# Kernel tuning notes

Measured on AMD Instinct MI355X. Metric: run time of the kernel, lower is better.

Reference implementation:

```python
import jax, jax.numpy as jnp
import numpy as np

DIM = 2048
N_HEADS = 16
HEAD_DIM = DIM // N_HEADS  # 128
HIDDEN = 8192
EPS = 1e-6
NEG = -1e9


def rmsnorm(x, w):
    xf = x.astype(jnp.float32)
    y = xf * jax.lax.rsqrt(jnp.mean(xf * xf, axis=-1, keepdims=True) + EPS)
    return y.astype(x.dtype) * w


def apply_rope(x, cos, sin):
    # x: [B,S,H,Hd]; cos/sin: [S,Hd//2] -> broadcast [1,S,1,Hd//2]
    xf = x.astype(jnp.float32)
    xr = xf[..., 0::2]
    xi = xf[..., 1::2]
    c = cos[None, :, None, :]
    s = sin[None, :, None, :]
    or_ = xr * c - xi * s
    oi_ = xr * s + xi * c
    out = jnp.stack([or_, oi_], axis=-1).reshape(x.shape)
    return out.astype(x.dtype)


def setup_inputs() -> dict:
    key = jax.random.key(0)
    ks = jax.random.split(key, 10)
    B, S = 1, 2048
    x = jax.random.normal(ks[0], (B, S, DIM), dtype=jnp.float32)
    # RoPE frequencies (Llama-style, theta=10000)
    inv_freq = 1.0 / (10000.0 ** (jnp.arange(0, HEAD_DIM, 2, dtype=jnp.float32) / HEAD_DIM))
    angles = jnp.arange(S, dtype=jnp.float32)[:, None] * inv_freq[None, :]  # [S, Hd//2]
    freqs_cos = jnp.cos(angles)
    freqs_sin = jnp.sin(angles)
    # causal additive mask [1,1,S,S]
    mask = jnp.where(jnp.tril(jnp.ones((S, S), dtype=bool)), 0.0, NEG).astype(jnp.float32)[None, None]
    sc = 0.02
    wq = jax.random.normal(ks[1], (DIM, DIM), dtype=jnp.float32) * sc
    wk = jax.random.normal(ks[2], (DIM, DIM), dtype=jnp.float32) * sc
    wv = jax.random.normal(ks[3], (DIM, DIM), dtype=jnp.float32) * sc
    wo = jax.random.normal(ks[4], (DIM, DIM), dtype=jnp.float32) * sc
    w1 = jax.random.normal(ks[5], (DIM, HIDDEN), dtype=jnp.float32) * sc
    w2 = jax.random.normal(ks[6], (HIDDEN, DIM), dtype=jnp.float32) * sc
    w3 = jax.random.normal(ks[7], (DIM, HIDDEN), dtype=jnp.float32) * sc
    attn_norm_w = jnp.ones((DIM,), dtype=jnp.float32)
    ffn_norm_w = jnp.ones((DIM,), dtype=jnp.float32)
    return {"x": x, "freqs_cos": freqs_cos, "freqs_sin": freqs_sin, "mask": mask,
            "wq": wq, "wk": wk, "wv": wv, "wo": wo, "w1": w1, "w2": w2, "w3": w3,
            "attn_norm_w": attn_norm_w, "ffn_norm_w": ffn_norm_w}


def reference(x, freqs_cos, freqs_sin, mask, wq, wk, wv, wo, w1, w2, w3, attn_norm_w, ffn_norm_w):
    B, S, D = x.shape
    # --- attention (pre-norm) ---
    hn = rmsnorm(x, attn_norm_w)
    q = (hn @ wq).reshape(B, S, N_HEADS, HEAD_DIM)
    k = (hn @ wk).reshape(B, S, N_HEADS, HEAD_DIM)
    v = (hn @ wv).reshape(B, S, N_HEADS, HEAD_DIM)
    q = apply_rope(q, freqs_cos, freqs_sin)
    k = apply_rope(k, freqs_cos, freqs_sin)
    scores = jnp.einsum('bqhd,bkhd->bhqk', q, k) / (HEAD_DIM ** 0.5) + mask
    attn = jax.nn.softmax(scores.astype(jnp.float32), axis=-1).astype(q.dtype)
    ctx = jnp.einsum('bhqk,bkhd->bqhd', attn, v).reshape(B, S, D)
    h = x + ctx @ wo
    # --- SwiGLU FFN (pre-norm) ---
    fn = rmsnorm(h, ffn_norm_w)
    ff = (jax.nn.silu(fn @ w1) * (fn @ w3)) @ w2
    return h + ff
```

## Files before the change

kernel.cpp:

```cpp
#include <hip/hip_runtime.h>
#include <hip/hip_bf16.h>

#define DIM 2048
#define HEAD_DIM 128
#define N_HEADS 16
#define SEQ 2048
#define HID 8192
#define SQKV 6144

typedef short bf16x8 __attribute__((ext_vector_type(8)));
typedef float f32x4 __attribute__((ext_vector_type(4)));
using bf16 = __hip_bfloat16;

#define MFMA16(a, b, c) __builtin_amdgcn_mfma_f32_16x16x32_bf16(a, b, c, 0, 0, 0)

__device__ __forceinline__ unsigned short f2bu(float f) {
    union { bf16 b; unsigned short u; } cv;
    cv.b = __float2bfloat16(f);
    return cv.u;
}

__device__ __forceinline__ void gl16(const void* g, void* l) {
    __builtin_amdgcn_global_load_lds(
        (const __attribute__((address_space(1))) unsigned int*)g,
        (__attribute__((address_space(3))) unsigned int*)l, 16, 0, 0);
}

__global__ __launch_bounds__(256) void rmsnorm_bf16_k(
    const float* __restrict__ x, const float* __restrict__ w, bf16* __restrict__ y)
{
    const int row = blockIdx.x;
    const int tid = threadIdx.x;
    const float* xr = x + (size_t)row * DIM;
    float4 v0 = ((const float4*)xr)[tid];
    float4 v1 = ((const float4*)xr)[tid + 256];
    float ss = v0.x*v0.x + v0.y*v0.y + v0.z*v0.z + v0.w*v0.w
             + v1.x*v1.x + v1.y*v1.y + v1.z*v1.z + v1.w*v1.w;
    for (int o = 32; o > 0; o >>= 1) ss += __shfl_down(ss, o);
    __shared__ float red[4];
    if ((tid & 63) == 0) red[tid >> 6] = ss;
    __syncthreads();
    float tot = red[0] + red[1] + red[2] + red[3];
    float r = rsqrtf(tot * (1.0f / DIM) + 1e-6f);
    float4 w0 = ((const float4*)w)[tid];
    float4 w1 = ((const float4*)w)[tid + 256];
    ushort4 o0, o1;
    o0.x = f2bu(v0.x * r * w0.x); o0.y = f2bu(v0.y * r * w0.y);
    o0.z = f2bu(v0.z * r * w0.z); o0.w = f2bu(v0.w * r * w0.w);
    o1.x = f2bu(v1.x * r * w1.x); o1.y = f2bu(v1.y * r * w1.y);
    o1.z = f2bu(v1.z * r * w1.z); o1.w = f2bu(v1.w * r * w1.w);
    ushort4* yr = (ushort4*)(y + (size_t)row * DIM);
    yr[tid] = o0;
    yr[tid + 256] = o1;
}

__global__ __launch_bounds__(256) void rmsnorm4_k(
    const float* __restrict__ part, const float* __restrict__ x,
    const float* __restrict__ w, float* __restrict__ hout, bf16* __restrict__ y)
{
    const int row = blockIdx.x;
    const int tid = threadIdx.x;
    const size_t base = (size_t)row * DIM;
    const size_t SP = (size_t)SEQ * DIM;
    float4 r0, r1;
    float ss = 0.0f;
    {
        float4 a  = ((const float4*)(x + base))[tid];
        float4 p0 = ((const float4*)(part + base))[tid];
        float4 p1 = ((const float4*)(part + SP + base))[tid];
        float4 p2 = ((const float4*)(part + 2 * SP + base))[tid];
        float4 p3 = ((const float4*)(part + 3 * SP + base))[tid];
        r0.x = a.x + ((p0.x + p1.x) + (p2.x + p3.x));
        r0.y = a.y + ((p0.y + p1.y) + (p2.y + p3.y));
        r0.z = a.z + ((p0.z + p1.z) + (p2.z + p3.z));
        r0.w = a.w + ((p0.w + p1.w) + (p2.w + p3.w));
        ((float4*)(hout + base))[tid] = r0;
        ss += r0.x*r0.x + r0.y*r0.y + r0.z*r0.z + r0.w*r0.w;
    }
    {
        const int t2 = tid + 256;
        float4 a  = ((const float4*)(x + base))[t2];
        float4 p0 = ((const float4*)(part + base))[t2];
        float4 p1 = ((const float4*)(part + SP + base))[t2];
        float4 p2 = ((const float4*)(part + 2 * SP + base))[t2];
        float4 p3 = ((const float4*)(part + 3 * SP + base))[t2];
        r1.x = a.x + ((p0.x + p1.x) + (p2.x + p3.x));
        r1.y = a.y + ((p0.y + p1.y) + (p2.y + p3.y));
        r1.z = a.z + ((p0.z + p1.z) + (p2.z + p3.z));
        r1.w = a.w + ((p0.w + p1.w) + (p2.w + p3.w));
        ((float4*)(hout + base))[t2] = r1;
        ss += r1.x*r1.x + r1.y*r1.y + r1.z*r1.z + r1.w*r1.w;
    }
    for (int o = 32; o > 0; o >>= 1) ss += __shfl_down(ss, o);
    __shared__ float red[4];
    if ((tid & 63) == 0) red[tid >> 6] = ss;
    __syncthreads();
    float tot = red[0] + red[1] + red[2] + red[3];
    float r = rsqrtf(tot * (1.0f / DIM) + 1e-6f);
    float4 w0 = ((const float4*)w)[tid];
    float4 w1 = ((const float4*)w)[tid + 256];
    ushort4 o0, o1;
    o0.x = f2bu(r0.x * r * w0.x); o0.y = f2bu(r0.y * r * w0.y);
    o0.z = f2bu(r0.z * r * w0.z); o0.w = f2bu(r0.w * r * w0.w);
    o1.x = f2bu(r1.x * r * w1.x); o1.y = f2bu(r1.y * r * w1.y);
    o1.z = f2bu(r1.z * r * w1.z); o1.w = f2bu(r1.w * r * w1.w);
    ushort4* yr = (ushort4*)(y + base);
    yr[tid] = o0;
    yr[tid + 256] = o1;
}

__global__ __launch_bounds__(256) void reduce4_k(
    const float* __restrict__ part, const float* __restrict__ h, float* __restrict__ out)
{
    const size_t i = (size_t)blockIdx.x * 256 + threadIdx.x;
    const size_t SP4 = (size_t)SEQ * DIM / 4;
    float4 a  = ((const float4*)h)[i];
    float4 p0 = ((const float4*)part)[i];
    float4 p1 = ((const float4*)part)[i + SP4];
    float4 p2 = ((const float4*)part)[i + 2 * SP4];
    float4 p3 = ((const float4*)part)[i + 3 * SP4];
    float4 r;
    r.x = a.x + ((p0.x + p1.x) + (p2.x + p3.x));
    r.y = a.y + ((p0.y + p1.y) + (p2.y + p3.y));
    r.z = a.z + ((p0.z + p1.z) + (p2.z + p3.z));
    r.w = a.w + ((p0.w + p1.w) + (p2.w + p3.w));
    ((float4*)out)[i] = r;
}

__global__ __launch_bounds__(256) void convT_f32_bf16_k(
    const float* __restrict__ in, bf16* __restrict__ out, int R, int C)
{
    __shared__ float t[32][33];
    const int tx = threadIdx.x, ty = threadIdx.y;
    const int x0 = blockIdx.x * 32, y0 = blockIdx.y * 32;
#pragma unroll
    for (int i = 0; i < 4; ++i)
        t[ty + i * 8][tx] = in[(size_t)(y0 + ty + i * 8) * C + x0 + tx];
    __syncthreads();
#pragma unroll
    for (int i = 0; i < 4; ++i)
        out[(size_t)(x0 + ty + i * 8) * R + y0 + tx] = __float2bfloat16(t[tx][ty + i * 8]);
}

__global__ __launch_bounds__(256) void convT3_f32_bf16_k(
    const float* __restrict__ wq, const float* __restrict__ wk,
    const float* __restrict__ wv, bf16* __restrict__ out)
{
    const int z = blockIdx.z;
    const float* in = z == 0 ? wq : (z == 1 ? wk : wv);
    bf16* o = out + (size_t)z * DIM * DIM;
    __shared__ float t[32][33];
    const int tx = threadIdx.x, ty = threadIdx.y;
    const int x0 = blockIdx.x * 32, y0 = blockIdx.y * 32;
#pragma unroll
    for (int i = 0; i < 4; ++i)
        t[ty + i * 8][tx] = in[(size_t)(y0 + ty + i * 8) * DIM + x0 + tx];
    __syncthreads();
#pragma unroll
    for (int i = 0; i < 4; ++i)
        o[(size_t)(x0 + ty + i * 8) * DIM + y0 + tx] = __float2bfloat16(t[tx][ty + i * 8]);
}

__global__ __launch_bounds__(256) void transpose_bf16_k(
    const bf16* __restrict__ in, int istride, bf16* __restrict__ out)
{
    __shared__ unsigned short t[32][33];
    const int tx = threadIdx.x, ty = threadIdx.y;
    const int x = blockIdx.x * 32 + tx;
    const int y0 = blockIdx.y * 32;
    const unsigned short* inu = (const unsigned short*)in;
    unsigned short* outu = (unsigned short*)out;
#pragma unroll
    for (int i = 0; i < 4; ++i)
        t[ty + i * 8][tx] = inu[(size_t)(y0 + ty + i * 8) * istride + x];
    __syncthreads();
    const int x2 = blockIdx.y * 32 + tx;
    const int y2 = blockIdx.x * 32;
#pragma unroll
    for (int i = 0; i < 4; ++i)
        outu[(size_t)(y2 + ty + i * 8) * SEQ + x2] = t[tx][ty + i * 8];
}

__global__ __launch_bounds__(256) void rope_qk_k(
    bf16* __restrict__ q, bf16* __restrict__ k,
    const float* __restrict__ cosb, const float* __restrict__ sinb)
{
    const int gid = blockIdx.x * 256 + threadIdx.x;
    const int s = gid >> 10;
    const int p = gid & 1023;
    const int h = p >> 6, j = p & 63;
    const size_t off = (size_t)s * SQKV + h * HEAD_DIM + 2 * j;
    const float c = cosb[s * 64 + j], sn = sinb[s * 64 + j];
    float xr = __bfloat162float(q[off]), xi = __bfloat162float(q[off + 1]);
    q[off]     = __float2bfloat16(xr * c - xi * sn);
    q[off + 1] = __float2bfloat16(xr * sn + xi * c);
    xr = __bfloat162float(k[off]); xi = __bfloat162float(k[off + 1]);
    k[off]     = __float2bfloat16(xr * c - xi * sn);
    k[off + 1] = __float2bfloat16(xr * sn + xi * c);
}

template <int EP>
__global__ __launch_bounds__(512, 1) void gemm256_k(
    const bf16* __restrict__ A, const bf16* __restrict__ Bt, const bf16* __restrict__ Bt2,
    bf16* __restrict__ Cb, float* __restrict__ Pf,
    int M, int N, int K, int gx, int ntile, int Ks)
{
    extern __shared__ char smem[];
    const int t512 = threadIdx.x;
    const int w = t512 >> 6, lane = t512 & 63;
    const int lr = lane & 15, lg = lane >> 4;
    const int wm = w >> 2, wn = w & 3;
    const int bofs = (wn & 1) * 64;
    const int swz = (lr & 7) << 4;

    const int nwg = gridDim.x;
    const int q8 = nwg >> 3, r8 = nwg & 7;
    const int xcd = blockIdx.x & 7, seqq = blockIdx.x >> 3;
    const int wgid = (xcd < r8 ? xcd * (q8 + 1) : r8 * (q8 + 1) + (xcd - r8) * q8) + seqq;
    const int split = wgid / ntile;
    const int tile = wgid % ntile;
    const int grp = tile / (4 * gx), rem = tile % (4 * gx);
    const int m0 = (grp * 4 + (rem & 3)) * 256, n0 = (rem >> 2) * 256;
    const int kb0 = split * Ks;
    const int niter = Ks >> 7;

    const bf16* aS[2][2]; const bf16* bS[2][2];
    int sOff[2];
#pragma unroll
    for (int c = 0; c < 2; ++c) {
        const int s = (c * 512 + t512) * 16;
        const int pp = s ^ (((s >> 7) & 7) << 4);
        const int row = pp >> 7, colE = (pp & 127) >> 1;
        sOff[c] = s;
#pragma unroll
        for (int hs = 0; hs < 2; ++hs) {
            aS[hs][c] = A + (size_t)(m0 + hs * 128 + row) * K + kb0 + colE;
            const int rg = n0 + hs * 128 + row;
            if (EP == 4) {
                const int g = rg >> 4;
                const bf16* src = (g & 1) ? Bt2 : Bt;
                const int j = ((g >> 1) << 4) + (rg & 15);
                bS[hs][c] = src + (size_t)j * K + kb0 + colE;
            } else {
                bS[hs][c] = Bt + (size_t)rg * K + kb0 + colE;
            }
        }
    }
    auto stA = [&](int buf, int kt, int hs) {
        char* base = smem + (buf * 2 + hs) * 16384;
        gl16(aS[hs][0] + (kt << 6), base + sOff[0]);
        gl16(aS[hs][1] + (kt << 6), base + sOff[1]);
    };
    auto stB = [&](int buf, int kt, int hs) {
        char* base = smem + 65536 + (buf * 2 + hs) * 16384;
        gl16(bS[hs][0] + (kt << 6), base + sOff[0]);
        gl16(bS[hs][1] + (kt << 6), base + sOff[1]);
    };

    const char* A0m = smem + (0 * 2 + wm) * 16384;
    const char* A1m = smem + (1 * 2 + wm) * 16384;
    const char* B0m = smem + 65536 + (0 * 2 + (wn >> 1)) * 16384;
    const char* B1m = smem + 65536 + (1 * 2 + (wn >> 1)) * 16384;

    f32x4 acc[8][4] = {};
    bf16x8 bfr[4][2];
    bf16x8 x0, x1, x2, x3;

#define SBAR __builtin_amdgcn_s_barrier()
#define LGKM0 do { asm volatile("s_waitcnt lgkmcnt(0)" ::: "memory"); \
                   __builtin_amdgcn_sched_barrier(0); } while (0)
#define WVM(n) do { asm volatile("s_waitcnt vmcnt(" #n ")" ::: "memory"); \
                    __builtin_amdgcn_sched_barrier(0); } while (0)
#define LDA4(base, mf0) do { \
    x0 = *(const bf16x8*)((base) + (((mf0) * 16 + lr) * 128) + ((lg * 16) ^ swz)); \
    x1 = *(const bf16x8*)((base) + (((mf0) * 16 + lr) * 128) + ((64 + lg * 16) ^ swz)); \
    x2 = *(const bf16x8*)((base) + ((((mf0) + 1) * 16 + lr) * 128) + ((lg * 16) ^ swz)); \
    x3 = *(const bf16x8*)((base) + ((((mf0) + 1) * 16 + lr) * 128) + ((64 + lg * 16) ^ swz)); \
    } while (0)
#define LDB8(base) do { \
    _Pragma("unroll") \
    for (int nf = 0; nf < 4; ++nf) { \
        bfr[nf][0] = *(const bf16x8*)((base) + ((bofs + nf * 16 + lr) * 128) + ((lg * 16) ^ swz)); \
        bfr[nf][1] = *(const bf16x8*)((base) + ((bofs + nf * 16 + lr) * 128) + ((64 + lg * 16) ^ swz)); \
    } } while (0)
#define MFMA_PH(mf0) do { \
    __builtin_amdgcn_s_setprio(1); \
    _Pragma("unroll") \
    for (int nf = 0; nf < 4; ++nf) { \
        acc[(mf0)][nf]     = MFMA16(x0, bfr[nf][0], acc[(mf0)][nf]); \
        acc[(mf0)][nf]     = MFMA16(x1, bfr[nf][1], acc[(mf0)][nf]); \
        acc[(mf0) + 1][nf] = MFMA16(x2, bfr[nf][0], acc[(mf0) + 1][nf]); \
        acc[(mf0) + 1][nf] = MFMA16(x3, bfr[nf][1], acc[(mf0) + 1][nf]); \
    } \
    __builtin_amdgcn_s_setprio(0); } while (0)

    stB(0, 0, 0); stB(0, 0, 1); stA(0, 0, 0); stA(0, 0, 1);
    stB(1, 1, 0); stB(1, 1, 1);
    WVM(4);
    SBAR;

    for (int t = 0; t < niter; ++t) {
        const bool pf = (t + 1 < niter);
        const int k1 = 2 * t + 1, k2 = 2 * t + 2, k3 = 2 * t + 3;

        LDB8(B0m);
        LDA4(A0m, 0);
        stA(1, k1, 0);
        SBAR; LGKM0; MFMA_PH(0); SBAR;
        LDA4(A0m, 2);
        stA(1, k1, 1);
        SBAR; LGKM0; MFMA_PH(2); SBAR;
        LDA4(A0m, 4);
        if (pf) stB(0, k2, 0);
        SBAR; LGKM0; MFMA_PH(4); SBAR;
        if (pf) { WVM(2); } else { WVM(0); }
        LDA4(A0m, 6);
        if (pf) stB(0, k2, 1);
        SBAR; LGKM0; MFMA_PH(6); SBAR;
        LDB8(B1m);
        LDA4(A1m, 0);
        if (pf) stA(0, k2, 0);
        SBAR; LGKM0; MFMA_PH(0); SBAR;
        LDA4(A1m, 2);
        if (pf) stA(0, k2, 1);
        SBAR; LGKM0; MFMA_PH(2); SBAR;
        LDA4(A1m, 4);
        if (pf) stB(1, k3, 0);
        SBAR; LGKM0; MFMA_PH(4); SBAR;
        if (pf) WVM(2);
        LDA4(A1m, 6);
        if (pf) stB(1, k3, 1);
        SBAR; LGKM0; MFMA_PH(6); SBAR;
    }
#undef SBAR
#undef LGKM0
#undef WVM
#undef LDA4
#undef LDB8
#undef MFMA_PH

    if (EP == 4) {
        const int jb = (n0 >> 1) + wn * 32;
        const int NH = N >> 1;
#pragma unroll
        for (int mf = 0; mf < 8; ++mf)
#pragma unroll
            for (int pp = 0; pp < 4; pp += 2) {
                const int row = m0 + wm * 128 + mf * 16 + lg * 4;
                const int j = jb + (pp >> 1) * 16 + lr;
#pragma unroll
                for (int r = 0; r < 4; ++r) {
                    const float a = acc[mf][pp][r];
                    const float b = acc[mf][pp + 1][r];
                    const float s = a / (1.0f + __expf(-a));
                    Cb[(size_t)(row + r) * NH + j] = __float2bfloat16(s * b);
                }
            }
    } else {
        float* pf_base = Pf + (size_t)split * M * N;
#pragma unroll
        for (int mf = 0; mf < 8; ++mf)
#pragma unroll
            for (int nf = 0; nf < 4; ++nf) {
                const int row = m0 + wm * 128 + mf * 16 + lg * 4;
                const int col = n0 + wn * 64 + nf * 16 + lr;
#pragma unroll
                for (int r = 0; r < 4; ++r) {
                    const size_t idx = (size_t)(row + r) * N + col;
                    const float v = acc[mf][nf][r];
                    if (EP == 0) Cb[idx] = __float2bfloat16(v);
                    else         pf_base[idx] = v;
                }
            }
    }
}

__global__ __launch_bounds__(256) void attn_fwd_k(
    const bf16* __restrict__ qkv, const bf16* __restrict__ vT, bf16* __restrict__ ctx)
{
    const int tid = threadIdx.x;
    const int w = tid >> 6, lane = tid & 63;
    const int lr = lane & 15, lg = lane >> 4;
    const int h = blockIdx.y;
    const int qidx = (blockIdx.y < 8) ? blockIdx.x : (31 - blockIdx.x);
    const int q0b = qidx * 64;
    const int nt = qidx + 1;

    __shared__ __align__(16) unsigned short Kt[2][64 * 128];
    __shared__ __align__(16) unsigned short Vt[2][128 * 64];
    __shared__ __align__(16) unsigned short Pp[4][16 * 64];

    const char* kbase = (const char*)(qkv + DIM + h * HEAD_DIM);
    const char* vbase = (const char*)(vT + (size_t)h * HEAD_DIM * SEQ);

    const int krow_c = tid >> 4;
    const int kcolB  = (tid & 15) * 16;
    const int vrow_c = tid >> 3;
    const int vcolB  = (tid & 7) * 16;

    auto stage = [&](int buf, int kb) {
#pragma unroll
        for (int c = 0; c < 4; ++c) {
            const int r = c * 16 + krow_c;
            gl16(kbase + (size_t)(kb + r) * (SQKV * 2) + (kcolB ^ ((r & 7) << 4)),
                 &Kt[buf][c * 2048 + tid * 8]);
        }
#pragma unroll
        for (int c = 0; c < 4; ++c) {
            const int r = c * 32 + vrow_c;
            gl16(vbase + (size_t)r * (SEQ * 2) + kb * 2 + (vcolB ^ ((r & 7) << 4)),
                 &Vt[buf][c * 2048 + tid * 8]);
        }
    };

    bf16x8 qf[4];
    const bf16* qrow = qkv + (size_t)(q0b + w * 16 + lr) * SQKV + h * HEAD_DIM;
#pragma unroll
    for (int dt = 0; dt < 4; ++dt)
        qf[dt] = *(const bf16x8*)(qrow + dt * 32 + lg * 8);

    f32x4 o[8] = {};
    float m[4], l[4];
#pragma unroll
    for (int j = 0; j < 4; ++j) { m[j] = -3e38f; l[j] = 0.0f; }
    const float scale = 0.08838834764831845f;

    stage(0, 0);
    __syncthreads();

    int cur = 0;
    for (int t = 0; t < nt; ++t) {
        const int kb = t * 64;
        if (t + 1 < nt) stage(cur ^ 1, kb + 64);

        f32x4 s[4] = {};
        __builtin_amdgcn_s_setprio(1);
#pragma unroll
        for (int ss = 0; ss < 4; ++ss) {
            const int r = ss * 16 + lr;
            const int sw = (r & 7) << 3;
#pragma unroll
            for (int dt = 0; dt < 4; ++dt) {
                bf16x8 kf = *(const bf16x8*)&Kt[cur][r * 128 + ((dt * 32 + lg * 8) ^ sw)];
                s[ss] = MFMA16(qf[dt], kf, s[ss]);
            }
        }
        __builtin_amdgcn_s_setprio(0);

        float al[4];
#pragma unroll
        for (int j = 0; j < 4; ++j) {
            const int qi = q0b + w * 16 + lg * 4 + j;
            const int prow = lg * 4 + j;
            const int psw = (prow & 7) << 3;
            float a[4];
#pragma unroll
            for (int ss = 0; ss < 4; ++ss)
                a[ss] = s[ss][j] * scale + ((kb + ss * 16 + lr) > qi ? -1e9f : 0.0f);
            float mx = fmaxf(fmaxf(a[0], a[1]), fmaxf(a[2], a[3]));
            mx = fmaxf(mx, __shfl_xor(mx, 1));
            mx = fmaxf(mx, __shfl_xor(mx, 2));
            mx = fmaxf(mx, __shfl_xor(mx, 4));
            mx = fmaxf(mx, __shfl_xor(mx, 8));
            const float mn = fmaxf(m[j], mx);
            const float asc = __expf(m[j] - mn);
            float e0 = __expf(a[0] - mn), e1 = __expf(a[1] - mn);
            float e2 = __expf(a[2] - mn), e3 = __expf(a[3] - mn);
            float rs = (e0 + e1) + (e2 + e3);
            rs += __shfl_xor(rs, 1); rs += __shfl_xor(rs, 2);
            rs += __shfl_xor(rs, 4); rs += __shfl_xor(rs, 8);
            l[j] = l[j] * asc + rs;
            m[j] = mn;
            al[j] = asc;
            Pp[w][prow * 64 + ((lr)      ^ psw)] = f2bu(e0);
            Pp[w][prow * 64 + ((16 + lr) ^ psw)] = f2bu(e1);
            Pp[w][prow * 64 + ((32 + lr) ^ psw)] = f2bu(e2);
            Pp[w][prow * 64 + ((48 + lr) ^ psw)] = f2bu(e3);
        }
#pragma unroll
        for (int d2 = 0; d2 < 8; ++d2)
#pragma unroll
            for (int j = 0; j < 4; ++j) o[d2][j] *= al[j];

        asm volatile("s_waitcnt lgkmcnt(0)" ::: "memory");
        __builtin_amdgcn_sched_barrier(0);
        const int asw = (lr & 7) << 3;
        bf16x8 pa0 = *(const bf16x8*)&Pp[w][lr * 64 + ((lg * 8)      ^ asw)];
        bf16x8 pa1 = *(const bf16x8*)&Pp[w][lr * 64 + ((32 + lg * 8) ^ asw)];

        __builtin_amdgcn_s_setprio(1);
#pragma unroll
        for (int d2 = 0; d2 < 8; ++d2) {
            const int rv = d2 * 16 + lr;
            const int vsw = (rv & 7) << 3;
            bf16x8 vf0 = *(const bf16x8*)&Vt[cur][rv * 64 + ((lg * 8)      ^ vsw)];
            bf16x8 vf1 = *(const bf16x8*)&Vt[cur][rv * 64 + ((32 + lg * 8) ^ vsw)];
            o[d2] = MFMA16(pa0, vf0, o[d2]);
            o[d2] = MFMA16(pa1, vf1, o[d2]);
        }
        __builtin_amdgcn_s_setprio(0);

        __syncthreads();
        cur ^= 1;
    }

#pragma unroll
    for (int j = 0; j < 4; ++j) {
        const float inv = 1.0f / l[j];
        bf16* dst = ctx + (size_t)(q0b + w * 16 + lg * 4 + j) * DIM + h * HEAD_DIM + lr;
#pragma unroll
        for (int d2 = 0; d2 < 8; ++d2)
            dst[d2 * 16] = __float2bfloat16(o[d2][j] * inv);
    }
}

extern "C" void kernel_launch(void* const* d_in, const int* in_sizes, int n_in,
                              void* d_out, int out_size, void* d_ws, size_t ws_size,
                              hipStream_t stream)
{
    const float* x   = (const float*)d_in[0];
    const float* fc  = (const float*)d_in[1];
    const float* fs  = (const float*)d_in[2];
    const float* wq  = (const float*)d_in[4];
    const float* wk  = (const float*)d_in[5];
    const float* wv  = (const float*)d_in[6];
    const float* wo  = (const float*)d_in[7];
    const float* w1  = (const float*)d_in[8];
    const float* w2  = (const float*)d_in[9];
    const float* w3  = (const float*)d_in[10];
    const float* anw = (const float*)d_in[11];
    const float* fnw = (const float*)d_in[12];
    float* out = (float*)d_out;

    char* p = (char*)d_ws;
    auto alloc = [&](size_t n) { char* r = p; p += (n + 255) & ~(size_t)255; return r; };
    bf16* wT  = (bf16*)alloc((size_t)HID * DIM * 2);
    bf16* hn  = (bf16*)alloc((size_t)SEQ * DIM * 2);
    bf16* qkv = (bf16*)alloc((size_t)SEQ * SQKV * 2);
    bf16* vt  = (bf16*)alloc((size_t)SEQ * DIM * 2);
    bf16* ctx = (bf16*)alloc((size_t)SEQ * DIM * 2);
    bf16* fn  = (bf16*)alloc((size_t)SEQ * DIM * 2);
    float* h  = (float*)alloc((size_t)SEQ * DIM * 4);
    bf16* g   = (bf16*)alloc((size_t)SEQ * HID * 2);
    float* sk = (float*)alloc((size_t)4 * SEQ * DIM * 4);
    bf16* w3T = hn;

    const dim3 tb32(32, 8);
    const int LDS256 = 131072;
    (void)hipFuncSetAttribute((const void*)gemm256_k<0>,
        hipFuncAttributeMaxDynamicSharedMemorySize, LDS256);
    (void)hipFuncSetAttribute((const void*)gemm256_k<3>,
        hipFuncAttributeMaxDynamicSharedMemorySize, LDS256);
    (void)hipFuncSetAttribute((const void*)gemm256_k<4>,
        hipFuncAttributeMaxDynamicSharedMemorySize, LDS256);

    rmsnorm_bf16_k<<<SEQ, 256, 0, stream>>>(x, anw, hn);

    convT3_f32_bf16_k<<<dim3(DIM / 32, DIM / 32, 3), tb32, 0, stream>>>(wq, wk, wv, wT);
    gemm256_k<0><<<(SEQ / 256) * (SQKV / 256), 512, LDS256, stream>>>(
        hn, wT, nullptr, qkv, nullptr, SEQ, SQKV, DIM, SQKV / 256, (SEQ / 256) * (SQKV / 256), DIM);

    rope_qk_k<<<(SEQ * 1024) / 256, 256, 0, stream>>>(qkv, qkv + DIM, fc, fs);
    transpose_bf16_k<<<dim3(DIM / 32, SEQ / 32), tb32, 0, stream>>>(qkv + 2 * DIM, SQKV, vt);

    attn_fwd_k<<<dim3(SEQ / 64, N_HEADS), 256, 0, stream>>>(qkv, vt, ctx);

    convT_f32_bf16_k<<<dim3(DIM / 32, DIM / 32), tb32, 0, stream>>>(wo, wT, DIM, DIM);
    gemm256_k<3><<<(SEQ / 256) * (DIM / 256) * 4, 512, LDS256, stream>>>(
        ctx, wT, nullptr, nullptr, sk, SEQ, DIM, DIM, DIM / 256, (SEQ / 256) * (DIM / 256), 512);
    rmsnorm4_k<<<SEQ, 256, 0, stream>>>(sk, x, fnw, h, fn);

    convT_f32_bf16_k<<<dim3(HID / 32, DIM / 32), tb32, 0, stream>>>(w1, wT, DIM, HID);
    convT_f32_bf16_k<<<dim3(HID / 32, DIM / 32), tb32, 0, stream>>>(w3, w3T, DIM, HID);
    gemm256_k<4><<<(SEQ / 256) * ((2 * HID) / 256), 512, LDS256, stream>>>(
        fn, wT, w3T, g, nullptr, SEQ, 2 * HID, DIM, (2 * HID) / 256,
        (SEQ / 256) * ((2 * HID) / 256), DIM);

    convT_f32_bf16_k<<<dim3(DIM / 32, HID / 32), tb32, 0, stream>>>(w2, wT, HID, DIM);
    gemm256_k<3><<<(SEQ / 256) * (DIM / 256) * 4, 512, LDS256, stream>>>(
        g, wT, nullptr, nullptr, sk, SEQ, DIM, HID, DIM / 256, (SEQ / 256) * (DIM / 256), 2048);
    reduce4_k<<<(SEQ * DIM / 4) / 256, 256, 0, stream>>>(sk, h, out);
}
```

Measured before the change: 491.4 us.

## Pair causal query tiles in one attention block to share K/V staging

The attention kernel now runs 512 threads per block. Two groups of four waves each take complementary query tiles (qidx and 31-qidx), so one block covers a balanced pair and the K/V tiles staged in LDS are shared by both. V is no longer double-buffered; it is loaded each iteration and waited on before the PV step, while K stays double-buffered. Waves whose tile is already finished idle through the barriers. Separately, the GEMM main loop gains a partial lgkmcnt(8) wait before the first barrier of each half-iteration.

```diff
diff --git a/kernel.cpp b/kernel.cpp
--- a/kernel.cpp
+++ b/kernel.cpp
@@ -269,6 +269,8 @@
 #define SBAR __builtin_amdgcn_s_barrier()
 #define LGKM0 do { asm volatile("s_waitcnt lgkmcnt(0)" ::: "memory"); \
                    __builtin_amdgcn_sched_barrier(0); } while (0)
+#define LGKM8 do { asm volatile("s_waitcnt lgkmcnt(8)" ::: "memory"); \
+                   __builtin_amdgcn_sched_barrier(0); } while (0)
 #define WVM(n) do { asm volatile("s_waitcnt vmcnt(" #n ")" ::: "memory"); \
                     __builtin_amdgcn_sched_barrier(0); } while (0)
 #define LDA4(base, mf0) do { \
@@ -306,6 +308,7 @@
         LDB8(B0m);
         LDA4(A0m, 0);
         stA(1, k1, 0);
+        LGKM8;
         SBAR; LGKM0; MFMA_PH(0); SBAR;
         LDA4(A0m, 2);
         stA(1, k1, 1);
@@ -320,6 +323,7 @@
         LDB8(B1m);
         LDA4(A1m, 0);
         if (pf) stA(0, k2, 0);
+        LGKM8;
         SBAR; LGKM0; MFMA_PH(0); SBAR;
         LDA4(A1m, 2);
         if (pf) stA(0, k2, 1);
@@ -334,6 +338,7 @@
     }
 #undef SBAR
 #undef LGKM0
+#undef LGKM8
 #undef WVM
 #undef LDA4
 #undef LDB8
@@ -375,20 +380,23 @@
     }
 }
 
-__global__ __launch_bounds__(256) void attn_fwd_k(
+__global__ __launch_bounds__(512) void attn_fwd_k(
     const bf16* __restrict__ qkv, const bf16* __restrict__ vT, bf16* __restrict__ ctx)
 {
     const int tid = threadIdx.x;
-    const int w = tid >> 6, lane = tid & 63;
+    const int w8 = tid >> 6, lane = tid & 63;
     const int lr = lane & 15, lg = lane >> 4;
+    const int w = w8 & 3, tsel = w8 >> 2;
     const int h = blockIdx.y;
-    const int qidx = (blockIdx.y < 8) ? blockIdx.x : (31 - blockIdx.x);
+    const int bx = blockIdx.x;
+    const int qidx = tsel ? (31 - bx) : bx;
     const int q0b = qidx * 64;
-    const int nt = qidx + 1;
+    const int myNt = qidx + 1;
+    const int nt = 32 - bx;
 
     __shared__ __align__(16) unsigned short Kt[2][64 * 128];
-    __shared__ __align__(16) unsigned short Vt[2][128 * 64];
-    __shared__ __align__(16) unsigned short Pp[4][16 * 64];
+    __shared__ __align__(16) unsigned short Vt[128 * 64];
+    __shared__ __align__(16) unsigned short Pp[8][16 * 64];
 
     const char* kbase = (const char*)(qkv + DIM + h * HEAD_DIM);
     const char* vbase = (const char*)(vT + (size_t)h * HEAD_DIM * SEQ);
@@ -398,20 +406,22 @@
     const int vrow_c = tid >> 3;
     const int vcolB  = (tid & 7) * 16;
 
-    auto stage = [&](int buf, int kb) {
-#pragma unroll
-        for (int c = 0; c < 4; ++c) {
-            const int r = c * 16 + krow_c;
+    auto stageK = [&](int buf, int kb) {
+#pragma unroll
+        for (int c = 0; c < 2; ++c) {
+            const int r = c * 32 + krow_c;
             gl16(kbase + (size_t)(kb + r) * (SQKV * 2) + (kcolB ^ ((r & 7) << 4)),
-                 &Kt[buf][c * 2048 + tid * 8]);
-        }
-#pragma unroll
-        for (int c = 0; c < 4; ++c) {
-            const int r = c * 32 + vrow_c;
-            gl16(vbase + (size_t)r * (SEQ * 2) + kb * 2 + (vcolB ^ ((r & 7) << 4)),
-                 &Vt[buf][c * 2048 + tid * 8]);
+                 &Kt[buf][c * 4096 + tid * 8]);
         }
     };
+    auto stageV = [&](int kb) {
+#pragma unroll
+        for (int c = 0; c < 2; ++c) {
+            const int r = c * 64 + vrow_c;
+            gl16(vbase + (size_t)r * (SEQ * 2) + kb * 2 + (vcolB ^ ((r & 7) << 4)),
+                 &Vt[c * 4096 + tid * 8]);
+        }
+    };
 
     bf16x8 qf[4];
     const bf16* qrow = qkv + (size_t)(q0b + w * 16 + lr) * SQKV + h * HEAD_DIM;
@@ -425,82 +435,96 @@
     for (int j = 0; j < 4; ++j) { m[j] = -3e38f; l[j] = 0.0f; }
     const float scale = 0.08838834764831845f;
 
-    stage(0, 0);
-    __syncthreads();
+    stageK(0, 0);
+    asm volatile("s_waitcnt vmcnt(0)" ::: "memory");
+    __builtin_amdgcn_sched_barrier(0);
+    __builtin_amdgcn_s_barrier();
 
     int cur = 0;
     for (int t = 0; t < nt; ++t) {
         const int kb = t * 64;
-        if (t + 1 < nt) stage(cur ^ 1, kb + 64);
-
-        f32x4 s[4] = {};
-        __builtin_amdgcn_s_setprio(1);
-#pragma unroll
-        for (int ss = 0; ss < 4; ++ss) {
-            const int r = ss * 16 + lr;
-            const int sw = (r & 7) << 3;
-#pragma unroll
-            for (int dt = 0; dt < 4; ++dt) {
-                bf16x8 kf = *(const bf16x8*)&Kt[cur][r * 128 + ((dt * 32 + lg * 8) ^ sw)];
-                s[ss] = MFMA16(qf[dt], kf, s[ss]);
+        const bool pf = (t + 1 < nt);
+        stageV(kb);
+        if (pf) stageK(cur ^ 1, kb + 64);
+        const bool act = (t < myNt);
+
+        if (act) {
+            f32x4 s[4] = {};
+            __builtin_amdgcn_s_setprio(1);
+#pragma unroll
+            for (int ss = 0; ss < 4; ++ss) {
+                const int r = ss * 16 + lr;
+                const int sw = (r & 7) << 3;
+#pragma unroll
+                for (int dt = 0; dt < 4; ++dt) {
+                    bf16x8 kf = *(const bf16x8*)&Kt[cur][r * 128 + ((dt * 32 + lg * 8) ^ sw)];
+                    s[ss] = MFMA16(qf[dt], kf, s[ss]);
+                }
             }
+            __builtin_amdgcn_s_setprio(0);
+
+            float al[4];
+#pragma unroll
+            for (int j = 0; j < 4; ++j) {
+                const int qi = q0b + w * 16 + lg * 4 + j;
+                const int prow = lg * 4 + j;
+                const int psw = (prow & 7) << 3;
+                float a[4];
+#pragma unroll
+                for (int ss = 0; ss < 4; ++ss)
+                    a[ss] = s[ss][j] * scale + ((kb + ss * 16 + lr) > qi ? -1e9f : 0.0f);
+                float mx = fmaxf(fmaxf(a[0], a[1]), fmaxf(a[2], a[3]));
+                mx = fmaxf(mx, __shfl_xor(mx, 1));
+                mx = fmaxf(mx, __shfl_xor(mx, 2));
+                mx = fmaxf(mx, __shfl_xor(mx, 4));
+                mx = fmaxf(mx, __shfl_xor(mx, 8));
+                const float mn = fmaxf(m[j], mx);
+                const float asc = __expf(m[j] - mn);
+                float e0 = __expf(a[0] - mn), e1 = __expf(a[1] - mn);
+                float e2 = __expf(a[2] - mn), e3 = __expf(a[3] - mn);
+                float rs = (e0 + e1) + (e2 + e3);
+                rs += __shfl_xor(rs, 1); rs += __shfl_xor(rs, 2);
+                rs += __shfl_xor(rs, 4); rs += __shfl_xor(rs, 8);
+                l[j] = l[j] * asc + rs;
+                m[j] = mn;
+                al[j] = asc;
+                Pp[w8][prow * 64 + ((lr)      ^ psw)] = f2bu(e0);
+                Pp[w8][prow * 64 + ((16 + lr) ^ psw)] = f2bu(e1);
+                Pp[w8][prow * 64 + ((32 + lr) ^ psw)] = f2bu(e2);
+                Pp[w8][prow * 64 + ((48 + lr) ^ psw)] = f2bu(e3);
+            }
+#pragma unroll
+            for (int d2 = 0; d2 < 8; ++d2)
+#pragma unroll
+                for (int j = 0; j < 4; ++j) o[d2][j] *= al[j];
         }
-        __builtin_amdgcn_s_setprio(0);
-
-        float al[4];
-#pragma unroll
-        for (int j = 0; j < 4; ++j) {
-            const int qi = q0b + w * 16 + lg * 4 + j;
-            const int prow = lg * 4 + j;
-            const int psw = (prow & 7) << 3;
-            float a[4];
-#pragma unroll
-            for (int ss = 0; ss < 4; ++ss)
-                a[ss] = s[ss][j] * scale + ((kb + ss * 16 + lr) > qi ? -1e9f : 0.0f);
-            float mx = fmaxf(fmaxf(a[0], a[1]), fmaxf(a[2], a[3]));
-            mx = fmaxf(mx, __shfl_xor(mx, 1));
-            mx = fmaxf(mx, __shfl_xor(mx, 2));
-            mx = fmaxf(mx, __shfl_xor(mx, 4));
-            mx = fmaxf(mx, __shfl_xor(mx, 8));
-            const float mn = fmaxf(m[j], mx);
-            const float asc = __expf(m[j] - mn);
-            float e0 = __expf(a[0] - mn), e1 = __expf(a[1] - mn);
-            float e2 = __expf(a[2] - mn), e3 = __expf(a[3] - mn);
-            float rs = (e0 + e1) + (e2 + e3);
-            rs += __shfl_xor(rs, 1); rs += __shfl_xor(rs, 2);
-            rs += __shfl_xor(rs, 4); rs += __shfl_xor(rs, 8);
-            l[j] = l[j] * asc + rs;
-            m[j] = mn;
-            al[j] = asc;
-            Pp[w][prow * 64 + ((lr)      ^ psw)] = f2bu(e0);
-            Pp[w][prow * 64 + ((16 + lr) ^ psw)] = f2bu(e1);
-            Pp[w][prow * 64 + ((32 + lr) ^ psw)] = f2bu(e2);
-            Pp[w][prow * 64 + ((48 + lr) ^ psw)] = f2bu(e3);
+
+        if (pf) { asm volatile("s_waitcnt vmcnt(2)" ::: "memory"); }
+        else    { asm volatile("s_waitcnt vmcnt(0)" ::: "memory"); }
+        __builtin_amdgcn_sched_barrier(0);
+        __builtin_amdgcn_s_barrier();
+
+        if (act) {
+            asm volatile("s_waitcnt lgkmcnt(0)" ::: "memory");
+            __builtin_amdgcn_sched_barrier(0);
+            const int asw = (lr & 7) << 3;
+            bf16x8 pa0 = *(const bf16x8*)&Pp[w8][lr * 64 + ((lg * 8)      ^ asw)];
+            bf16x8 pa1 = *(const bf16x8*)&Pp[w8][lr * 64 + ((32 + lg * 8) ^ asw)];
+
+            __builtin_amdgcn_s_setprio(1);
+#pragma unroll
+            for (int d2 = 0; d2 < 8; ++d2) {
+                const int rv = d2 * 16 + lr;
+                const int vsw = (rv & 7) << 3;
+                bf16x8 vf0 = *(const bf16x8*)&Vt[rv * 64 + ((lg * 8)      ^ vsw)];
+                bf16x8 vf1 = *(const bf16x8*)&Vt[rv * 64 + ((32 + lg * 8) ^ vsw)];
+                o[d2] = MFMA16(pa0, vf0, o[d2]);
+                o[d2] = MFMA16(pa1, vf1, o[d2]);
+            }
+            __builtin_amdgcn_s_setprio(0);
         }
-#pragma unroll
-        for (int d2 = 0; d2 < 8; ++d2)
-#pragma unroll
-            for (int j = 0; j < 4; ++j) o[d2][j] *= al[j];
-
-        asm volatile("s_waitcnt lgkmcnt(0)" ::: "memory");
-        __builtin_amdgcn_sched_barrier(0);
-        const int asw = (lr & 7) << 3;
-        bf16x8 pa0 = *(const bf16x8*)&Pp[w][lr * 64 + ((lg * 8)      ^ asw)];
-        bf16x8 pa1 = *(const bf16x8*)&Pp[w][lr * 64 + ((32 + lg * 8) ^ asw)];
-
-        __builtin_amdgcn_s_setprio(1);
-#pragma unroll
-        for (int d2 = 0; d2 < 8; ++d2) {
-            const int rv = d2 * 16 + lr;
-            const int vsw = (rv & 7) << 3;
-            bf16x8 vf0 = *(const bf16x8*)&Vt[cur][rv * 64 + ((lg * 8)      ^ vsw)];
-            bf16x8 vf1 = *(const bf16x8*)&Vt[cur][rv * 64 + ((32 + lg * 8) ^ vsw)];
-            o[d2] = MFMA16(pa0, vf0, o[d2]);
-            o[d2] = MFMA16(pa1, vf1, o[d2]);
-        }
-        __builtin_amdgcn_s_setprio(0);
-
-        __syncthreads();
+
+        __builtin_amdgcn_s_barrier();
         cur ^= 1;
     }
 
@@ -563,7 +587,7 @@
     rope_qk_k<<<(SEQ * 1024) / 256, 256, 0, stream>>>(qkv, qkv + DIM, fc, fs);
     transpose_bf16_k<<<dim3(DIM / 32, SEQ / 32), tb32, 0, stream>>>(qkv + 2 * DIM, SQKV, vt);
 
-    attn_fwd_k<<<dim3(SEQ / 64, N_HEADS), 256, 0, stream>>>(qkv, vt, ctx);
+    attn_fwd_k<<<dim3(16, N_HEADS), 512, 0, stream>>>(qkv, vt, ctx);
 
     convT_f32_bf16_k<<<dim3(DIM / 32, DIM / 32), tb32, 0, stream>>>(wo, wT, DIM, DIM);
     gemm256_k<3><<<(SEQ / 256) * (DIM / 256) * 4, 512, LDS256, stream>>>(
```

After: 477.0 us. 2.9% less time.
